# Kernel tuning notes

Hardware: AMD Instinct MI355X
Metric: run time of the kernel (lower is better)

Reference implementation:

```python
import jax, jax.numpy as jnp
import numpy as np

N_NODES = 500_000
N_EDGES = 16_000_000


def setup_inputs() -> dict:
    key = jax.random.key(0)
    ks = jax.random.split(key, 8)
    x = jax.random.normal(ks[0], (N_NODES, 6), dtype=jnp.float32)
    edge_index = jax.random.randint(ks[1], (2, N_EDGES), 0, N_NODES, dtype=jnp.int64)
    conv_w = jax.random.normal(ks[2], (4, 6), dtype=jnp.float32) * 0.4
    conv_b = jax.random.normal(ks[3], (4,), dtype=jnp.float32) * 0.1
    fc1_w = jax.random.normal(ks[4], (64, 4), dtype=jnp.float32) * 0.5
    fc1_b = jax.random.normal(ks[5], (64,), dtype=jnp.float32) * 0.1
    fc3_w = jax.random.normal(ks[6], (10, 64), dtype=jnp.float32) * 0.125
    fc3_b = jax.random.normal(ks[7], (10,), dtype=jnp.float32) * 0.1
    return {"x": x, "edge_index": edge_index, "conv_w": conv_w, "conv_b": conv_b,
            "fc1_w": fc1_w, "fc1_b": fc1_b, "fc3_w": fc3_w, "fc3_b": fc3_b}


def reference(x, edge_index, conv_w, conv_b, fc1_w, fc1_b, fc3_w, fc3_b):
    n = x.shape[0]
    loop = jnp.arange(n, dtype=edge_index.dtype)
    # PyG GCNConv default: add self-loops, symmetric normalization
    row = jnp.concatenate([edge_index[0], loop])  # source
    col = jnp.concatenate([edge_index[1], loop])  # target (aggregation index)
    deg = jax.ops.segment_sum(jnp.ones_like(col, dtype=x.dtype), col, num_segments=n)
    dinv = jnp.where(deg > 0, deg ** -0.5, 0.0).astype(x.dtype)
    norm = dinv[row] * dinv[col]                  # [E+N]
    h = x @ conv_w.T                              # [N, 4]
    msg = h[row] * norm[:, None]                  # gather + scale
    agg = jax.ops.segment_sum(msg, col, num_segments=n) + conv_b  # scatter-add
    t = jnp.tanh(agg)
    # F.dropout treated as identity (deterministic eval reference)
    g = jnp.mean(t, axis=0, keepdims=True)        # global_mean_pool, batch=None -> [1, 4]
    hdn = jax.nn.relu(g @ fc1_w.T + fc1_b)
    out = hdn @ fc3_w.T + fc3_b                   # [1, output_size]
    return out
```

## Files before the change

kernel.cpp:

```cpp
#include <hip/hip_runtime.h>
#include <math.h>


constexpr int NP = 1024;
constexpr int SHIFT = 10;
constexpr unsigned MASK = 1023;
constexpr int NPART_MAX = 512;
constexpr int EPB = 8192;
constexpr int BINB = 512;


__global__ __launch_bounds__(BINB) void k_bin(const int* __restrict__ row,
                                              const int* __restrict__ col, int E,
                                              int P, int cap, int* __restrict__ cursor,
                                              unsigned* __restrict__ binned) {
    __shared__ unsigned lbuf[EPB];
    __shared__ int lcount[NPART_MAX];
    __shared__ int lbase[NPART_MAX];
    __shared__ int gbase[NPART_MAX];
    __shared__ int lpos[NPART_MAX];
    __shared__ int sc[NPART_MAX];

    int t = threadIdx.x;
    int start = blockIdx.x * EPB;
    int end = min(start + EPB, E);

    for (int i = t; i < NPART_MAX; i += BINB) { lcount[i] = 0; lpos[i] = 0; }
    __syncthreads();

    for (int e = start + t; e < end; e += BINB)
        atomicAdd(&lcount[col[e] >> SHIFT], 1);
    __syncthreads();

    sc[t] = lcount[t];
    __syncthreads();
    for (int off = 1; off < NPART_MAX; off <<= 1) {
        int v = (t >= off) ? sc[t - off] : 0;
        __syncthreads();
        sc[t] += v;
        __syncthreads();
    }
    lbase[t] = sc[t] - lcount[t];
    if (t < P) {
        int c = lcount[t];
        gbase[t] = (c > 0) ? atomicAdd(&cursor[t], c) : 0;
    }
    __syncthreads();

    for (int e = start + t; e < end; e += BINB) {
        int r = row[e];
        int c = col[e];
        int part = c >> SHIFT;
        int slot = atomicAdd(&lpos[part], 1);
        lbuf[lbase[part] + slot] = ((unsigned)r << SHIFT) | ((unsigned)c & MASK);
    }
    __syncthreads();

    int lane = t & 63;
    int wave = t >> 6;
    const int nwaves = BINB / 64;
    for (int part = wave; part < P; part += nwaves) {
        int cnt = lcount[part];
        if (cnt == 0) continue;
        int lb = lbase[part];
        int gb = gbase[part];
        unsigned* dst = binned + (size_t)part * cap;
        for (int j = lane; j < cnt; j += 64) {
            int slot = gb + j;
            if (slot < cap) dst[slot] = lbuf[lb + j];
        }
    }
}

__global__ __launch_bounds__(1024) void k_part_node(const unsigned* __restrict__ binned,
                                                    const int* __restrict__ cursor, int cap,
                                                    const float* __restrict__ x,
                                                    const float* __restrict__ conv_w, int n,
                                                    float4* __restrict__ p4,
                                                    float* __restrict__ dinvg) {
    __shared__ int degs[NP];
    __shared__ float w[24];
    int part = blockIdx.x;
    int tid = threadIdx.x;
    if (tid < 24) w[tid] = conv_w[tid];
    if (tid < NP) degs[tid] = 0;
    __syncthreads();
    int cnt = min(cursor[part], cap);
    const unsigned* bin = binned + (size_t)part * cap;
    for (int e = tid; e < cnt; e += 1024)
        atomicAdd(&degs[bin[e] & MASK], 1);
    __syncthreads();
    int base = part * NP;
    int node = base + tid;
    if (tid < NP && node < n) {
        float dinv = rsqrtf((float)(degs[tid] + 1));
        const float* xr = x + (size_t)node * 6;
        float2 a = *(const float2*)xr;
        float2 b = *(const float2*)(xr + 2);
        float2 cc = *(const float2*)(xr + 4);
        float xv[6] = {a.x, a.y, b.x, b.y, cc.x, cc.y};
        float h0 = 0.f, h1 = 0.f, h2 = 0.f, h3 = 0.f;
#pragma unroll
        for (int j = 0; j < 6; ++j) {
            h0 += xv[j] * w[j];
            h1 += xv[j] * w[6 + j];
            h2 += xv[j] * w[12 + j];
            h3 += xv[j] * w[18 + j];
        }
        float4 o;
        o.x = h0 * dinv; o.y = h1 * dinv; o.z = h2 * dinv; o.w = h3 * dinv;
        p4[node] = o;
        dinvg[node] = dinv;
    }
}

__global__ __launch_bounds__(1024) void k_acc(const unsigned* __restrict__ binned,
                                              const int* __restrict__ cursor, int cap,
                                              const float4* __restrict__ p4,
                                              const float* __restrict__ dinvg,
                                              const float* __restrict__ conv_b, int n,
                                              float* __restrict__ gsum) {
    __shared__ float S[NP * 4];
    __shared__ float4 red[16];
    int part = blockIdx.x;
    int tid = threadIdx.x;
    for (int i = tid; i < NP * 4; i += 1024) S[i] = 0.f;
    __syncthreads();
    int cnt = min(cursor[part], cap);
    const unsigned* bin = binned + (size_t)part * cap;
    for (int e = tid; e < cnt; e += 1024) {
        unsigned v = bin[e];
        float4 pv = p4[v >> SHIFT];
        int local = (int)(v & MASK);
        atomicAdd(&S[local * 4 + 0], pv.x);
        atomicAdd(&S[local * 4 + 1], pv.y);
        atomicAdd(&S[local * 4 + 2], pv.z);
        atomicAdd(&S[local * 4 + 3], pv.w);
    }
    __syncthreads();
    float b0 = conv_b[0], b1 = conv_b[1], b2 = conv_b[2], b3 = conv_b[3];
    float4 acc = {0.f, 0.f, 0.f, 0.f};
    int node = part * NP + tid;
    if (tid < NP && node < n) {
        float di = dinvg[node];
        float4 pv = p4[node];
        acc.x = tanhf(di * (S[tid * 4 + 0] + pv.x) + b0);
        acc.y = tanhf(di * (S[tid * 4 + 1] + pv.y) + b1);
        acc.z = tanhf(di * (S[tid * 4 + 2] + pv.z) + b2);
        acc.w = tanhf(di * (S[tid * 4 + 3] + pv.w) + b3);
    }
#pragma unroll
    for (int off = 32; off > 0; off >>= 1) {
        acc.x += __shfl_down(acc.x, off);
        acc.y += __shfl_down(acc.y, off);
        acc.z += __shfl_down(acc.z, off);
        acc.w += __shfl_down(acc.w, off);
    }
    int lane = tid & 63, wv = tid >> 6;
    if (lane == 0) red[wv] = acc;
    __syncthreads();
    if (tid == 0) {
        float4 tt = red[0];
        for (int k = 1; k < 16; ++k) {
            tt.x += red[k].x; tt.y += red[k].y; tt.z += red[k].z; tt.w += red[k].w;
        }
        unsafeAtomicAdd(&gsum[0], tt.x);
        unsafeAtomicAdd(&gsum[1], tt.y);
        unsafeAtomicAdd(&gsum[2], tt.z);
        unsafeAtomicAdd(&gsum[3], tt.w);
    }
}

__global__ void k_head(const float* __restrict__ gsum,
                       const float* __restrict__ fc1w, const float* __restrict__ fc1b,
                       const float* __restrict__ fc3w, const float* __restrict__ fc3b,
                       float* __restrict__ out, int n) {
    __shared__ float hdn[64];
    int t = threadIdx.x;
    float g[4];
    float inv_n = 1.0f / (float)n;
#pragma unroll
    for (int j = 0; j < 4; ++j) g[j] = gsum[j] * inv_n;
    if (t < 64) {
        float a = fc1b[t];
#pragma unroll
        for (int j = 0; j < 4; ++j) a += g[j] * fc1w[t * 4 + j];
        hdn[t] = fmaxf(a, 0.f);
    }
    __syncthreads();
    if (t < 10) {
        float a = fc3b[t];
#pragma unroll
        for (int k = 0; k < 64; ++k) a += hdn[k] * fc3w[t * 64 + k];
        out[t] = a;
    }
}


__global__ void k_deg(const int* __restrict__ col, int n_edges, int* __restrict__ deg) {
    int t = blockIdx.x * blockDim.x + threadIdx.x;
    int base = t * 4;
    if (base + 4 <= n_edges) {
        int4 c = *(const int4*)(col + base);
        atomicAdd(&deg[c.x], 1); atomicAdd(&deg[c.y], 1);
        atomicAdd(&deg[c.z], 1); atomicAdd(&deg[c.w], 1);
    } else {
        for (int e = base; e < n_edges; ++e) atomicAdd(&deg[col[e]], 1);
    }
}

__global__ void k_node(const float* __restrict__ x, const float* __restrict__ conv_w,
                       const int* __restrict__ deg, float4* __restrict__ p, int n) {
    int i = blockIdx.x * blockDim.x + threadIdx.x;
    if (i >= n) return;
    const float* xr = x + (size_t)i * 6;
    float2 a = *(const float2*)xr;
    float2 b = *(const float2*)(xr + 2);
    float2 c = *(const float2*)(xr + 4);
    float xv[6] = {a.x, a.y, b.x, b.y, c.x, c.y};
    float dinv = rsqrtf((float)(deg[i] + 1));
    float h0 = 0.f, h1 = 0.f, h2 = 0.f, h3 = 0.f;
#pragma unroll
    for (int j = 0; j < 6; ++j) {
        h0 += xv[j] * conv_w[j];
        h1 += xv[j] * conv_w[6 + j];
        h2 += xv[j] * conv_w[12 + j];
        h3 += xv[j] * conv_w[18 + j];
    }
    float4 o; o.x = h0 * dinv; o.y = h1 * dinv; o.z = h2 * dinv; o.w = h3 * dinv;
    p[i] = o;
}

__global__ void k_scatter(const int* __restrict__ row, const int* __restrict__ col, int n_edges,
                          const float4* __restrict__ p, float* __restrict__ S) {
    int t = blockIdx.x * blockDim.x + threadIdx.x;
    int base = t * 2;
    if (base + 2 <= n_edges) {
        int2 r = *(const int2*)(row + base);
        int2 c = *(const int2*)(col + base);
        float4 p0 = p[r.x], p1 = p[r.y];
        float* s0 = S + 4 * c.x;
        unsafeAtomicAdd(s0 + 0, p0.x); unsafeAtomicAdd(s0 + 1, p0.y);
        unsafeAtomicAdd(s0 + 2, p0.z); unsafeAtomicAdd(s0 + 3, p0.w);
        float* s1 = S + 4 * c.y;
        unsafeAtomicAdd(s1 + 0, p1.x); unsafeAtomicAdd(s1 + 1, p1.y);
        unsafeAtomicAdd(s1 + 2, p1.z); unsafeAtomicAdd(s1 + 3, p1.w);
    } else {
        for (int e = base; e < n_edges; ++e) {
            int r = row[e], c = col[e];
            float4 pv = p[r];
            float* s = S + 4 * c;
            unsafeAtomicAdd(s + 0, pv.x); unsafeAtomicAdd(s + 1, pv.y);
            unsafeAtomicAdd(s + 2, pv.z); unsafeAtomicAdd(s + 3, pv.w);
        }
    }
}

__global__ void k_reduce(const float4* __restrict__ S4, const float4* __restrict__ p,
                         const int* __restrict__ deg, const float* __restrict__ conv_b,
                         int n, float* __restrict__ gsum) {
    int i = blockIdx.x * blockDim.x + threadIdx.x;
    float4 v = {0.f, 0.f, 0.f, 0.f};
    if (i < n) {
        float dinv = rsqrtf((float)(deg[i] + 1));
        float4 s = S4[i];
        float4 pp = p[i];
        v.x = tanhf(dinv * (s.x + pp.x) + conv_b[0]);
        v.y = tanhf(dinv * (s.y + pp.y) + conv_b[1]);
        v.z = tanhf(dinv * (s.z + pp.z) + conv_b[2]);
        v.w = tanhf(dinv * (s.w + pp.w) + conv_b[3]);
    }
#pragma unroll
    for (int off = 32; off > 0; off >>= 1) {
        v.x += __shfl_down(v.x, off);
        v.y += __shfl_down(v.y, off);
        v.z += __shfl_down(v.z, off);
        v.w += __shfl_down(v.w, off);
    }
    __shared__ float4 lds[4];
    int lane = threadIdx.x & 63, w = threadIdx.x >> 6;
    if (lane == 0) lds[w] = v;
    __syncthreads();
    if (threadIdx.x == 0) {
        float4 tt = lds[0];
        for (int k = 1; k < 4; ++k) {
            tt.x += lds[k].x; tt.y += lds[k].y; tt.z += lds[k].z; tt.w += lds[k].w;
        }
        unsafeAtomicAdd(&gsum[0], tt.x); unsafeAtomicAdd(&gsum[1], tt.y);
        unsafeAtomicAdd(&gsum[2], tt.z); unsafeAtomicAdd(&gsum[3], tt.w);
    }
}


extern "C" void kernel_launch(void* const* d_in, const int* in_sizes, int n_in,
                              void* d_out, int out_size, void* d_ws, size_t ws_size,
                              hipStream_t stream) {
    const float* x      = (const float*)d_in[0];
    const int*   ei     = (const int*)d_in[1];
    const float* conv_w = (const float*)d_in[2];
    const float* conv_b = (const float*)d_in[3];
    const float* fc1w   = (const float*)d_in[4];
    const float* fc1b   = (const float*)d_in[5];
    const float* fc3w   = (const float*)d_in[6];
    const float* fc3b   = (const float*)d_in[7];

    int n = in_sizes[0] / 6;
    int E = in_sizes[1] / 2;
    const int* row = ei;
    const int* col = ei + E;

    int P = (n + NP - 1) / NP;
    int avg = (E + P - 1) / P;
    int cap = ((avg + avg / 8 + 2048) + 15) & ~15;

    size_t off = 0;
    size_t cursor_off = off;          off += (size_t)P * sizeof(int);
    off = (off + 15) & ~(size_t)15;
    size_t gsum_off = off;            off += 4 * sizeof(float);
    size_t zero_end = off;
    off = (off + 15) & ~(size_t)15;
    size_t dinv_off = off;            off += (size_t)n * sizeof(float);
    off = (off + 15) & ~(size_t)15;
    size_t p_off = off;               off += (size_t)n * sizeof(float4);
    off = (off + 15) & ~(size_t)15;
    size_t bin_off = off;             off += (size_t)P * cap * sizeof(unsigned);
    size_t need = off;

    char* ws = (char*)d_ws;
    bool use_bin = (ws_size >= need) && (P <= NPART_MAX) && (n < (1 << 22));

    if (use_bin) {
        int* cursor = (int*)(ws + cursor_off);
        float* gsum = (float*)(ws + gsum_off);
        float* dinvg = (float*)(ws + dinv_off);
        float4* p4 = (float4*)(ws + p_off);
        unsigned* binned = (unsigned*)(ws + bin_off);

        hipMemsetAsync(d_ws, 0, zero_end, stream);
        int bin_blocks = (E + EPB - 1) / EPB;
        k_bin<<<bin_blocks, BINB, 0, stream>>>(row, col, E, P, cap, cursor, binned);
        k_part_node<<<P, 1024, 0, stream>>>(binned, cursor, cap, x, conv_w, n, p4, dinvg);
        k_acc<<<P, 1024, 0, stream>>>(binned, cursor, cap, p4, dinvg, conv_b, n, gsum);
        k_head<<<1, 64, 0, stream>>>(gsum, fc1w, fc1b, fc3w, fc3b, (float*)d_out, n);
    } else {
        size_t o = 0;
        int* deg = (int*)(ws + o);      o += (size_t)n * sizeof(int);
        o = (o + 15) & ~(size_t)15;
        float* S = (float*)(ws + o);    o += (size_t)n * 4 * sizeof(float);
        float* gsum = (float*)(ws + o);
        size_t zend = o + 4 * sizeof(float);
        o = (zend + 15) & ~(size_t)15;
        float4* p = (float4*)(ws + o);

        hipMemsetAsync(d_ws, 0, zend, stream);
        int t1 = (E + 3) / 4;
        k_deg<<<(t1 + 255) / 256, 256, 0, stream>>>(col, E, deg);
        k_node<<<(n + 255) / 256, 256, 0, stream>>>(x, conv_w, deg, p, n);
        int t3 = (E + 1) / 2;
        k_scatter<<<(t3 + 255) / 256, 256, 0, stream>>>(row, col, E, p, S);
        k_reduce<<<(n + 255) / 256, 256, 0, stream>>>((const float4*)S, p, deg, conv_b, n, gsum);
        k_head<<<1, 64, 0, stream>>>(gsum, fc1w, fc1b, fc3w, fc3b, (float*)d_out, n);
    }
}
```

Measured before the change: 668.2 us.

## Store scaled node features as fp16, vectorize edge loads, pad shared accumulators

Result: faster. 624.5 us (-6.5%).

```diff
diff --git a/kernel.cpp b/kernel.cpp
--- a/kernel.cpp
+++ b/kernel.cpp
@@ -1,4 +1,5 @@
 #include <hip/hip_runtime.h>
+#include <hip/hip_fp16.h>
 #include <math.h>
 
 
@@ -8,6 +9,9 @@
 constexpr int NPART_MAX = 512;
 constexpr int EPB = 8192;
 constexpr int BINB = 512;
+constexpr int BT = 512;
+
+struct alignas(8) Half4 { __half2 a, b; };
 
 
 __global__ __launch_bounds__(BINB) void k_bin(const int* __restrict__ row,
@@ -24,12 +28,25 @@
     int t = threadIdx.x;
     int start = blockIdx.x * EPB;
     int end = min(start + EPB, E);
-
-    for (int i = t; i < NPART_MAX; i += BINB) { lcount[i] = 0; lpos[i] = 0; }
-    __syncthreads();
-
-    for (int e = start + t; e < end; e += BINB)
-        atomicAdd(&lcount[col[e] >> SHIFT], 1);
+    bool full = (end - start) == EPB;
+
+    lcount[t] = 0; lpos[t] = 0;
+    __syncthreads();
+
+    if (full) {
+        const int4* c4 = (const int4*)(col + start);
+#pragma unroll
+        for (int i = 0; i < EPB / 4 / BINB; ++i) {
+            int4 c = c4[t + i * BINB];
+            atomicAdd(&lcount[c.x >> SHIFT], 1);
+            atomicAdd(&lcount[c.y >> SHIFT], 1);
+            atomicAdd(&lcount[c.z >> SHIFT], 1);
+            atomicAdd(&lcount[c.w >> SHIFT], 1);
+        }
+    } else {
+        for (int e = start + t; e < end; e += BINB)
+            atomicAdd(&lcount[col[e] >> SHIFT], 1);
+    }
     __syncthreads();
 
     sc[t] = lcount[t];
@@ -47,12 +64,30 @@
     }
     __syncthreads();
 
-    for (int e = start + t; e < end; e += BINB) {
-        int r = row[e];
-        int c = col[e];
-        int part = c >> SHIFT;
-        int slot = atomicAdd(&lpos[part], 1);
-        lbuf[lbase[part] + slot] = ((unsigned)r << SHIFT) | ((unsigned)c & MASK);
+    if (full) {
+        const int4* c4 = (const int4*)(col + start);
+        const int4* r4 = (const int4*)(row + start);
+#pragma unroll
+        for (int i = 0; i < EPB / 4 / BINB; ++i) {
+            int4 c = c4[t + i * BINB];
+            int4 r = r4[t + i * BINB];
+            int part, slot;
+            part = c.x >> SHIFT; slot = atomicAdd(&lpos[part], 1);
+            lbuf[lbase[part] + slot] = ((unsigned)r.x << SHIFT) | ((unsigned)c.x & MASK);
+            part = c.y >> SHIFT; slot = atomicAdd(&lpos[part], 1);
+            lbuf[lbase[part] + slot] = ((unsigned)r.y << SHIFT) | ((unsigned)c.y & MASK);
+            part = c.z >> SHIFT; slot = atomicAdd(&lpos[part], 1);
+            lbuf[lbase[part] + slot] = ((unsigned)r.z << SHIFT) | ((unsigned)c.z & MASK);
+            part = c.w >> SHIFT; slot = atomicAdd(&lpos[part], 1);
+            lbuf[lbase[part] + slot] = ((unsigned)r.w << SHIFT) | ((unsigned)c.w & MASK);
+        }
+    } else {
+        for (int e = start + t; e < end; e += BINB) {
+            int r = row[e], c = col[e];
+            int part = c >> SHIFT;
+            int slot = atomicAdd(&lpos[part], 1);
+            lbuf[lbase[part] + slot] = ((unsigned)r << SHIFT) | ((unsigned)c & MASK);
+        }
     }
     __syncthreads();
 
@@ -72,28 +107,38 @@
     }
 }
 
-__global__ __launch_bounds__(1024) void k_part_node(const unsigned* __restrict__ binned,
-                                                    const int* __restrict__ cursor, int cap,
-                                                    const float* __restrict__ x,
-                                                    const float* __restrict__ conv_w, int n,
-                                                    float4* __restrict__ p4,
-                                                    float* __restrict__ dinvg) {
+__global__ __launch_bounds__(BT) void k_part_node(const unsigned* __restrict__ binned,
+                                                  const int* __restrict__ cursor, int cap,
+                                                  const float* __restrict__ x,
+                                                  const float* __restrict__ conv_w, int n,
+                                                  Half4* __restrict__ ph,
+                                                  float* __restrict__ dinvg) {
     __shared__ int degs[NP];
     __shared__ float w[24];
     int part = blockIdx.x;
     int tid = threadIdx.x;
     if (tid < 24) w[tid] = conv_w[tid];
-    if (tid < NP) degs[tid] = 0;
+    for (int i = tid; i < NP; i += BT) degs[i] = 0;
     __syncthreads();
     int cnt = min(cursor[part], cap);
     const unsigned* bin = binned + (size_t)part * cap;
-    for (int e = tid; e < cnt; e += 1024)
+    const uint4* bin4 = (const uint4*)bin;
+    int cnt4 = cnt >> 2;
+    for (int i = tid; i < cnt4; i += BT) {
+        uint4 v = bin4[i];
+        atomicAdd(&degs[v.x & MASK], 1);
+        atomicAdd(&degs[v.y & MASK], 1);
+        atomicAdd(&degs[v.z & MASK], 1);
+        atomicAdd(&degs[v.w & MASK], 1);
+    }
+    for (int e = (cnt4 << 2) + tid; e < cnt; e += BT)
         atomicAdd(&degs[bin[e] & MASK], 1);
     __syncthreads();
     int base = part * NP;
-    int node = base + tid;
-    if (tid < NP && node < n) {
-        float dinv = rsqrtf((float)(degs[tid] + 1));
+    for (int i = tid; i < NP; i += BT) {
+        int node = base + i;
+        if (node >= n) continue;
+        float dinv = rsqrtf((float)(degs[i] + 1));
         const float* xr = x + (size_t)node * 6;
         float2 a = *(const float2*)xr;
         float2 b = *(const float2*)(xr + 2);
@@ -107,47 +152,67 @@
             h2 += xv[j] * w[12 + j];
             h3 += xv[j] * w[18 + j];
         }
-        float4 o;
-        o.x = h0 * dinv; o.y = h1 * dinv; o.z = h2 * dinv; o.w = h3 * dinv;
-        p4[node] = o;
+        Half4 o;
+        o.a = __floats2half2_rn(h0 * dinv, h1 * dinv);
+        o.b = __floats2half2_rn(h2 * dinv, h3 * dinv);
+        ph[node] = o;
         dinvg[node] = dinv;
     }
 }
 
-__global__ __launch_bounds__(1024) void k_acc(const unsigned* __restrict__ binned,
-                                              const int* __restrict__ cursor, int cap,
-                                              const float4* __restrict__ p4,
-                                              const float* __restrict__ dinvg,
-                                              const float* __restrict__ conv_b, int n,
-                                              float* __restrict__ gsum) {
-    __shared__ float S[NP * 4];
-    __shared__ float4 red[16];
+__global__ __launch_bounds__(BT) void k_acc(const unsigned* __restrict__ binned,
+                                            const int* __restrict__ cursor, int cap,
+                                            const Half4* __restrict__ ph,
+                                            const float* __restrict__ dinvg,
+                                            const float* __restrict__ conv_b, int n,
+                                            float* __restrict__ gsum) {
+    __shared__ float S[NP * 5];
+    __shared__ float4 red[BT / 64];
     int part = blockIdx.x;
     int tid = threadIdx.x;
-    for (int i = tid; i < NP * 4; i += 1024) S[i] = 0.f;
+    for (int i = tid; i < NP * 5; i += BT) S[i] = 0.f;
     __syncthreads();
     int cnt = min(cursor[part], cap);
     const unsigned* bin = binned + (size_t)part * cap;
-    for (int e = tid; e < cnt; e += 1024) {
+    const uint4* bin4 = (const uint4*)bin;
+    int cnt4 = cnt >> 2;
+    for (int i = tid; i < cnt4; i += BT) {
+        uint4 v = bin4[i];
+        Half4 h0 = ph[v.x >> SHIFT];
+        Half4 h1 = ph[v.y >> SHIFT];
+        Half4 h2 = ph[v.z >> SHIFT];
+        Half4 h3 = ph[v.w >> SHIFT];
+        float2 a, b; float* s;
+        a = __half22float2(h0.a); b = __half22float2(h0.b); s = &S[(v.x & MASK) * 5];
+        atomicAdd(s + 0, a.x); atomicAdd(s + 1, a.y); atomicAdd(s + 2, b.x); atomicAdd(s + 3, b.y);
+        a = __half22float2(h1.a); b = __half22float2(h1.b); s = &S[(v.y & MASK) * 5];
+        atomicAdd(s + 0, a.x); atomicAdd(s + 1, a.y); atomicAdd(s + 2, b.x); atomicAdd(s + 3, b.y);
+        a = __half22float2(h2.a); b = __half22float2(h2.b); s = &S[(v.z & MASK) * 5];
+        atomicAdd(s + 0, a.x); atomicAdd(s + 1, a.y); atomicAdd(s + 2, b.x); atomicAdd(s + 3, b.y);
+        a = __half22float2(h3.a); b = __half22float2(h3.b); s = &S[(v.w & MASK) * 5];
+        atomicAdd(s + 0, a.x); atomicAdd(s + 1, a.y); atomicAdd(s + 2, b.x); atomicAdd(s + 3, b.y);
+    }
+    for (int e = (cnt4 << 2) + tid; e < cnt; e += BT) {
         unsigned v = bin[e];
-        float4 pv = p4[v >> SHIFT];
-        int local = (int)(v & MASK);
-        atomicAdd(&S[local * 4 + 0], pv.x);
-        atomicAdd(&S[local * 4 + 1], pv.y);
-        atomicAdd(&S[local * 4 + 2], pv.z);
-        atomicAdd(&S[local * 4 + 3], pv.w);
+        Half4 h = ph[v >> SHIFT];
+        float2 a = __half22float2(h.a), b = __half22float2(h.b);
+        float* s = &S[(v & MASK) * 5];
+        atomicAdd(s + 0, a.x); atomicAdd(s + 1, a.y); atomicAdd(s + 2, b.x); atomicAdd(s + 3, b.y);
     }
     __syncthreads();
     float b0 = conv_b[0], b1 = conv_b[1], b2 = conv_b[2], b3 = conv_b[3];
     float4 acc = {0.f, 0.f, 0.f, 0.f};
-    int node = part * NP + tid;
-    if (tid < NP && node < n) {
+    int base = part * NP;
+    for (int i = tid; i < NP; i += BT) {
+        int node = base + i;
+        if (node >= n) continue;
         float di = dinvg[node];
-        float4 pv = p4[node];
-        acc.x = tanhf(di * (S[tid * 4 + 0] + pv.x) + b0);
-        acc.y = tanhf(di * (S[tid * 4 + 1] + pv.y) + b1);
-        acc.z = tanhf(di * (S[tid * 4 + 2] + pv.z) + b2);
-        acc.w = tanhf(di * (S[tid * 4 + 3] + pv.w) + b3);
+        Half4 hp = ph[node];
+        float2 pa = __half22float2(hp.a), pb = __half22float2(hp.b);
+        acc.x += tanhf(di * (S[i * 5 + 0] + pa.x) + b0);
+        acc.y += tanhf(di * (S[i * 5 + 1] + pa.y) + b1);
+        acc.z += tanhf(di * (S[i * 5 + 2] + pb.x) + b2);
+        acc.w += tanhf(di * (S[i * 5 + 3] + pb.y) + b3);
     }
 #pragma unroll
     for (int off = 32; off > 0; off >>= 1) {
@@ -161,7 +226,7 @@
     __syncthreads();
     if (tid == 0) {
         float4 tt = red[0];
-        for (int k = 1; k < 16; ++k) {
+        for (int k = 1; k < BT / 64; ++k) {
             tt.x += red[k].x; tt.y += red[k].y; tt.z += red[k].z; tt.w += red[k].w;
         }
         unsafeAtomicAdd(&gsum[0], tt.x);
@@ -321,7 +386,7 @@
     off = (off + 15) & ~(size_t)15;
     size_t dinv_off = off;            off += (size_t)n * sizeof(float);
     off = (off + 15) & ~(size_t)15;
-    size_t p_off = off;               off += (size_t)n * sizeof(float4);
+    size_t ph_off = off;              off += (size_t)n * sizeof(Half4);
     off = (off + 15) & ~(size_t)15;
     size_t bin_off = off;             off += (size_t)P * cap * sizeof(unsigned);
     size_t need = off;
@@ -333,14 +398,14 @@
         int* cursor = (int*)(ws + cursor_off);
         float* gsum = (float*)(ws + gsum_off);
         float* dinvg = (float*)(ws + dinv_off);
-        float4* p4 = (float4*)(ws + p_off);
+        Half4* ph = (Half4*)(ws + ph_off);
         unsigned* binned = (unsigned*)(ws + bin_off);
 
         hipMemsetAsync(d_ws, 0, zero_end, stream);
         int bin_blocks = (E + EPB - 1) / EPB;
         k_bin<<<bin_blocks, BINB, 0, stream>>>(row, col, E, P, cap, cursor, binned);
-        k_part_node<<<P, 1024, 0, stream>>>(binned, cursor, cap, x, conv_w, n, p4, dinvg);
-        k_acc<<<P, 1024, 0, stream>>>(binned, cursor, cap, p4, dinvg, conv_b, n, gsum);
+        k_part_node<<<P, BT, 0, stream>>>(binned, cursor, cap, x, conv_w, n, ph, dinvg);
+        k_acc<<<P, BT, 0, stream>>>(binned, cursor, cap, ph, dinvg, conv_b, n, gsum);
         k_head<<<1, 64, 0, stream>>>(gsum, fc1w, fc1b, fc3w, fc3b, (float*)d_out, n);
     } else {
         size_t o = 0;
```
